# Optimization experiments

Hardware: AMD Instinct MI355X
Metric: run time of the kernel (lower is better)

The kernel has to match this reference:

```python
import jax, jax.numpy as jnp
import numpy as np

B, T, NI, NH, NO = 32, 2048, 1, 512, 1


def setup_inputs() -> dict:
    key = jax.random.key(0)
    ks = jax.random.split(key, 7)
    x = jax.random.normal(ks[0], (B, T, NI), dtype=jnp.float32)
    # torch code draws h_0 ~ U[-1,1) once and tiles over batch; here per-batch uniform
    h_0 = jax.random.uniform(ks[1], (B, NH), dtype=jnp.float32) * 2.0 - 1.0
    w_input_std = 1.0 / np.sqrt(NH)
    W_ih = jax.random.normal(ks[2], (NH, NI), dtype=jnp.float32) * w_input_std
    prob_c = 0.1
    w_hidden_std = 1.5 / np.sqrt(prob_c * NH)
    mask = jax.random.bernoulli(ks[3], prob_c, (NH, NH)).astype(jnp.float32)
    W_hh = jax.random.normal(ks[4], (NH, NH), dtype=jnp.float32) * w_hidden_std * mask
    W_hz = jax.random.normal(ks[5], (NO, NH), dtype=jnp.float32) * w_input_std
    W_zh = jax.random.uniform(ks[6], (NH, NO), dtype=jnp.float32, minval=-1.0, maxval=1.0)
    return {"x": x, "h_0": h_0, "W_ih": W_ih, "W_hh": W_hh, "W_hz": W_hz, "W_zh": W_zh}


def reference(x, h_0, W_ih, W_hh, W_hz, W_zh):
    dt, tau = 0.001, 0.01
    alpha = dt / tau  # 0.1
    # precompute input projection for all timesteps: [T, B, NH]
    x_proj = jnp.einsum('bti,hi->tbh', x, W_ih)

    def step(carry, xp_t):
        h_prev, z_prev = carry  # [B,NH], [B,NO]
        h_transfer = jnp.tanh(h_prev)
        dhdt = -h_prev + h_transfer @ W_hh.T + xp_t + z_prev @ W_zh.T
        h_t = h_prev + alpha * dhdt
        z_t = jnp.tanh(h_t) @ W_hz.T
        return (h_t, z_t), (h_t, z_t)

    z0 = jnp.tanh(h_0) @ W_hz.T
    _, (h, z) = jax.lax.scan(step, (h_0, z0), x_proj)
    # scan stacks time first -> [T,B,*]; transpose to [B,T,*]
    return jnp.swapaxes(z, 0, 1), jnp.swapaxes(h, 0, 1)
```

## Files before the change

### kernel.cpp

```cpp
#include <hip/hip_runtime.h>


#define NH   512
#define TT   2048
#define BB   32
#define PAD  96
#define PIN  64

__global__ __launch_bounds__(512) void count_nnz(
    const float* __restrict__ Whh, int* __restrict__ nnz) {
  const int wib  = threadIdx.x >> 6;
  const int lane = threadIdx.x & 63;
  const int row  = blockIdx.x * 8 + wib;
  const float* wrow = Whh + (size_t)row * NH;
  int cnt = 0;
  for (int c = 0; c < NH / 64; ++c)
    cnt += __popcll(__ballot(wrow[c * 64 + lane] != 0.0f));
  if (lane == 0) nnz[row] = cnt;
}

__global__ __launch_bounds__(512) void sort_rows(
    const int* __restrict__ nnz, int* __restrict__ perm) {
  __shared__ int nl[NH];
  const int j = threadIdx.x;
  const int my = nnz[j];
  nl[j] = my;
  __syncthreads();
  int r = 0;
  const int4* p4 = (const int4*)nl;
  for (int i = 0; i < NH / 4; ++i) {
    int4 v = p4[i];
    const int base = i * 4;
    r += (v.x > my) || (v.x == my && base + 0 < j);
    r += (v.y > my) || (v.y == my && base + 1 < j);
    r += (v.z > my) || (v.z == my && base + 2 < j);
    r += (v.w > my) || (v.w == my && base + 3 < j);
  }
  perm[r] = j;
}

__global__ __launch_bounds__(64) void build_schedule(
    const float* __restrict__ Whh, const int* __restrict__ perm,
    float* __restrict__ vals, unsigned* __restrict__ offs,
    int* __restrict__ cntw) {
  __shared__ int cnt[2][32];
  const int lane = threadIdx.x;
  const int wid  = blockIdx.x;
  const int p    = wid * 64 + lane;
  const int half = lane >> 5;
  const int home = lane & 31;
  const int row  = perm[p];
  const float* wrow = Whh + (size_t)row * NH;

  unsigned occ32[16];
  int remaining = 0;
  unsigned nonempty = 0;
  #pragma unroll
  for (int r = 0; r < 16; ++r) {
    unsigned lo = 0, hi = 0;
    #pragma unroll
    for (int m = 0; m < 16; ++m) {
      lo |= (wrow[(2 * r)     + 32 * m] != 0.f) ? (1u << m) : 0u;
      hi |= (wrow[(2 * r + 1) + 32 * m] != 0.f) ? (1u << m) : 0u;
    }
    occ32[r] = lo | (hi << 16);
    remaining += __popc(lo) + __popc(hi);
    if (lo) nonempty |= 1u << (2 * r);
    if (hi) nonempty |= 1u << (2 * r + 1);
  }

  int s = 0;
  while (__ballot(remaining > 0) != 0ull && s < PAD) {
    cnt[half][home] = 0;
    __builtin_amdgcn_wave_barrier();

    bool placed = false;
    int  mybank = 0;
    unsigned excl = 0;

    for (int round = 0; round < 10; ++round) {
      const int cap = (round < 3) ? 1 : 2;
      if (round == 3) excl = 0;
      unsigned cand = (placed || remaining == 0) ? 0u : (nonempty & ~excl);
      bool want = cand != 0u;
      int bl = 0;
      if (want) {
        unsigned rot = home ? ((cand >> home) | (cand << (32 - home))) : cand;
        bl = (home + __ffs(rot) - 1) & 31;
      }
      if (__ballot(want) == 0ull) break;
      if (want) {
        int old = atomicAdd(&cnt[half][bl], 1);
        if (old < cap) { placed = true; mybank = bl; }
        else { atomicSub(&cnt[half][bl], 1); excl |= 1u << bl; }
      }
      __builtin_amdgcn_wave_barrier();
    }

    if (!placed && remaining > 0 && (PAD - s) <= remaining) {
      placed = true;
      mybank = __ffs(nonempty) - 1;
    }

    float v = 0.f; unsigned col = 0u;
    if (placed) {
      #pragma unroll
      for (int r = 0; r < 16; ++r) {
        if (r == (mybank >> 1)) {
          unsigned w   = occ32[r];
          unsigned m16 = (mybank & 1) ? (w >> 16) : (w & 0xFFFFu);
          int m = __ffs(m16) - 1;
          col = (unsigned)(mybank + 32 * m);
          unsigned nm = m16 & (m16 - 1u);
          occ32[r] = (mybank & 1) ? ((w & 0x0000FFFFu) | (nm << 16))
                                  : ((w & 0xFFFF0000u) | nm);
          if (nm == 0u) nonempty &= ~(1u << mybank);
        }
      }
      v = wrow[col];
      --remaining;
    }
    vals[s * NH + p] = v;
    offs[s * NH + p] = col;
    ++s;
  }
  if (lane == 0) cntw[wid] = s;
  for (int e = s; e < PAD; ++e) {
    vals[e * NH + p] = 0.f;
    offs[e * NH + p] = 0u;
  }
}

template <int CTRL, int RM>
__device__ __forceinline__ float dppadd(float v) {
  int t = __builtin_amdgcn_update_dpp(0, __float_as_int(v), CTRL, RM, 0xF, true);
  return v + __int_as_float(t);
}
__device__ __forceinline__ float wave_sum_lane63(float v) {
  v = dppadd<0xB1,  0xF>(v);
  v = dppadd<0x4E,  0xF>(v);
  v = dppadd<0x141, 0xF>(v);
  v = dppadd<0x140, 0xF>(v);
  v = dppadd<0x142, 0xA>(v);
  v = dppadd<0x143, 0xC>(v);
  return v;
}

__device__ __forceinline__ float ftanh(float x) {
  float xc = fminf(9.0f, fmaxf(-9.0f, x));
  float t  = __expf(2.0f * xc);
  return (t - 1.0f) * __builtin_amdgcn_rcpf(t + 1.0f);
}

#define GA(T_RD, E) (*(const float*)((const char*)(T_RD) + cidx[E]))

#define ESN_STEP(T_RD, T_WR, RWR, SIDX)                                      \
  {                                                                          \
    float d0 = 0.f, d1 = 0.f, d2 = 0.f, d3 = 0.f;                            \
    _Pragma("unroll")                                                        \
    for (int e = 0; e < PAD; e += 4) {                                       \
      if (e < cw) {                                                          \
        d0 = fmaf(wval[e + 0], GA(T_RD, e + 0), d0);                         \
        d1 = fmaf(wval[e + 1], GA(T_RD, e + 1), d1);                         \
        d2 = fmaf(wval[e + 2], GA(T_RD, e + 2), d2);                         \
        d3 = fmaf(wval[e + 3], GA(T_RD, e + 3), d3);                         \
      }                                                                      \
    }                                                                        \
    float dot  = (d0 + d1) + (d2 + d3);                                      \
    float xp   = x_lds[SIDX] * w_ih;                                         \
    float dhdt = ((dot - h) + xp) + z_prev * w_zh;                           \
    float hn   = h + 0.1f * dhdt;                                            \
    float thn  = ftanh(hn);                                                  \
    T_WR[row] = thn;                                                         \
    oh[(SIDX) * NH + row] = hn;                                              \
    float pzs = wave_sum_lane63(thn * w_hz);                                 \
    if (lane == 63) red[RWR][wid] = pzs;                                     \
    asm volatile("s_waitcnt lgkmcnt(0)\n\ts_barrier" ::: "memory");          \
    float4 r0 = *(const float4*)&red[RWR][0];                                \
    float4 r1 = *(const float4*)&red[RWR][4];                                \
    float z = ((r0.x + r0.y) + (r0.z + r0.w)) + ((r1.x + r1.y) + (r1.z + r1.w)); \
    if (p == 0) oz[SIDX] = z;                                                \
    z_prev = z; h = hn;                                                      \
  }

__global__ __launch_bounds__(512, 2) void esn_steps(
    const float* __restrict__ x,   const float* __restrict__ h0,
    const float* __restrict__ Wih, const float* __restrict__ Whz,
    const float* __restrict__ Wzh, const float* __restrict__ vals,
    const unsigned* __restrict__ offs, const int* __restrict__ perm,
    const int* __restrict__ cntw, float* __restrict__ out) {
  __shared__ float t_lds[2][NH];
  __shared__ float x_lds[TT];
  __shared__ __align__(16) float red[2][8];

  const int p    = threadIdx.x;
  const int b    = blockIdx.x;
  const int lane = p & 63;
  const int wid  = p >> 6;
  const int row  = perm[p];

  float* t0 = t_lds[0];
  float* t1 = t_lds[1];

  for (int i = p; i < TT; i += NH) x_lds[i] = x[(size_t)b * TT + i];

  int cw = __builtin_amdgcn_readfirstlane((cntw[wid] + 3) & ~3);

  float    wval[PAD];
  unsigned cidx[PAD];
  #pragma unroll
  for (int e = 0; e < PAD; ++e) {
    wval[e] = vals[e * NH + p];
    cidx[e] = offs[e * NH + p] * 4u;
  }
  #pragma unroll
  for (int e = 0; e < PIN; ++e)
    asm volatile("" : "+v"(wval[e]), "+v"(cidx[e]));

  const float w_ih = Wih[row];
  const float w_hz = Whz[row];
  const float w_zh = Wzh[row];
  float h = h0[(size_t)b * NH + row];

  float* oz = out + (size_t)b * TT;
  float* oh = out + (size_t)BB * TT + (size_t)b * TT * NH;

  float th0 = ftanh(h);
  t0[row] = th0;
  float pz = wave_sum_lane63(th0 * w_hz);
  if (lane == 63) red[0][wid] = pz;
  __syncthreads();
  float4 i0 = *(const float4*)&red[0][0];
  float4 i1 = *(const float4*)&red[0][4];
  float z_prev = ((i0.x + i0.y) + (i0.z + i0.w)) + ((i1.x + i1.y) + (i1.z + i1.w));

  for (int s = 0; s < TT; s += 2) {
    ESN_STEP(t0, t1, 1, s);
    ESN_STEP(t1, t0, 0, s + 1);
  }
}

extern "C" void kernel_launch(void* const* d_in, const int* in_sizes, int n_in,
                              void* d_out, int out_size, void* d_ws,
                              size_t ws_size, hipStream_t stream) {
  const float* x   = (const float*)d_in[0];
  const float* h0  = (const float*)d_in[1];
  const float* Wih = (const float*)d_in[2];
  const float* Whh = (const float*)d_in[3];
  const float* Whz = (const float*)d_in[4];
  const float* Wzh = (const float*)d_in[5];
  float* out = (float*)d_out;

  float*    vals = (float*)d_ws;
  unsigned* offs = (unsigned*)(vals + PAD * NH);
  int*      nnz  = (int*)(offs + PAD * NH);
  int*      perm = nnz + NH;
  int*      cntw = perm + NH;

  hipLaunchKernelGGL(count_nnz, dim3(NH / 8), dim3(512), 0, stream, Whh, nnz);
  hipLaunchKernelGGL(sort_rows, dim3(1), dim3(512), 0, stream, nnz, perm);
  hipLaunchKernelGGL(build_schedule, dim3(8), dim3(64), 0, stream,
                     Whh, perm, vals, offs, cntw);
  hipLaunchKernelGGL(esn_steps, dim3(BB), dim3(512), 0, stream,
                     x, h0, Wih, Whz, Wzh, vals, offs, perm, cntw, out);
}
```

Measured before the change: 2.795 ms.

## Split each batch recurrence across four workgroups with tagged global exchange

Each batch element is now handled by four 128-thread workgroups, each owning two waves' worth of rows, instead of one 512-thread block. The tanh state and partial z sums are exchanged through global memory each step using tag-stamped 64-bit relaxed atomics with spin-polling and double buffering. Block indices are mapped so that the four workgroups of a batch land on the same XCD. The intent is to spread the per-step dot-product work over more CUs and lower per-step latency, at the cost of a cross-workgroup global-memory handshake every step. Correctness depends on all 128 workgroups being co-resident, and the buffers are not reset between calls.

New measurement: 4.421 ms. +58.2%, slower.

```diff
diff --git a/kernel.cpp b/kernel.cpp
--- a/kernel.cpp
+++ b/kernel.cpp
@@ -4,8 +4,12 @@
 #define NH   512
 #define TT   2048
 #define BB   32
+#define SQ   4
+#define TPB  128
 #define PAD  96
-#define PIN  64
+#define PIN  96
+
+typedef unsigned long long u64;
 
 __global__ __launch_bounds__(512) void count_nnz(
     const float* __restrict__ Whh, int* __restrict__ nnz) {
@@ -152,59 +156,76 @@
   return (t - 1.0f) * __builtin_amdgcn_rcpf(t + 1.0f);
 }
 
+__device__ __forceinline__ u64 aload(u64* p) {
+  return __hip_atomic_load(p, __ATOMIC_RELAXED, __HIP_MEMORY_SCOPE_AGENT);
+}
+__device__ __forceinline__ void astore(u64* p, u64 v) {
+  __hip_atomic_store(p, v, __ATOMIC_RELAXED, __HIP_MEMORY_SCOPE_AGENT);
+}
+
 #define GA(T_RD, E) (*(const float*)((const char*)(T_RD) + cidx[E]))
 
-#define ESN_STEP(T_RD, T_WR, RWR, SIDX)                                      \
+#define EXCHANGE(TB, ZQ, TAG, DO_OZ, SIDX)                                   \
   {                                                                          \
-    float d0 = 0.f, d1 = 0.f, d2 = 0.f, d3 = 0.f;                            \
-    _Pragma("unroll")                                                        \
-    for (int e = 0; e < PAD; e += 4) {                                       \
-      if (e < cw) {                                                          \
-        d0 = fmaf(wval[e + 0], GA(T_RD, e + 0), d0);                         \
-        d1 = fmaf(wval[e + 1], GA(T_RD, e + 1), d1);                         \
-        d2 = fmaf(wval[e + 2], GA(T_RD, e + 2), d2);                         \
-        d3 = fmaf(wval[e + 3], GA(T_RD, e + 3), d3);                         \
-      }                                                                      \
+    asm volatile("s_waitcnt lgkmcnt(0)\n\ts_barrier" ::: "memory");          \
+    if (t == 0)                                                              \
+      astore((ZQ) + q, ((u64)(TAG) << 32) |                                  \
+                       (u64)__float_as_uint(red[0] + red[1]));               \
+    u64 v0=0, v1=0, v2=0, v3=0, vz=0;                                        \
+    bool o0=false, o1=false, o2=false, o3=false, ok_z = (t >= 4);            \
+    for (;;) {                                                               \
+      if (!o0)   v0 = aload((TB) + t);                                       \
+      if (!o1)   v1 = aload((TB) + t + 128);                                 \
+      if (!o2)   v2 = aload((TB) + t + 256);                                 \
+      if (!o3)   v3 = aload((TB) + t + 384);                                 \
+      if (!ok_z) vz = aload((ZQ) + t);                                       \
+      o0 = (unsigned)(v0 >> 32) == (TAG);                                    \
+      o1 = (unsigned)(v1 >> 32) == (TAG);                                    \
+      o2 = (unsigned)(v2 >> 32) == (TAG);                                    \
+      o3 = (unsigned)(v3 >> 32) == (TAG);                                    \
+      ok_z = ok_z || ((unsigned)(vz >> 32) == (TAG));                        \
+      if (o0 & o1 & o2 & o3 & ok_z) break;                                   \
     }                                                                        \
-    float dot  = (d0 + d1) + (d2 + d3);                                      \
-    float xp   = x_lds[SIDX] * w_ih;                                         \
-    float dhdt = ((dot - h) + xp) + z_prev * w_zh;                           \
-    float hn   = h + 0.1f * dhdt;                                            \
-    float thn  = ftanh(hn);                                                  \
-    T_WR[row] = thn;                                                         \
-    oh[(SIDX) * NH + row] = hn;                                              \
-    float pzs = wave_sum_lane63(thn * w_hz);                                 \
-    if (lane == 63) red[RWR][wid] = pzs;                                     \
+    tl[t]       = __uint_as_float((unsigned)v0);                             \
+    tl[t + 128] = __uint_as_float((unsigned)v1);                             \
+    tl[t + 256] = __uint_as_float((unsigned)v2);                             \
+    tl[t + 384] = __uint_as_float((unsigned)v3);                             \
+    if (w == 0) {                                                            \
+      float zv = (t < 4) ? __uint_as_float((unsigned)vz) : 0.0f;             \
+      float zz = (__shfl(zv, 0) + __shfl(zv, 1)) +                           \
+                 (__shfl(zv, 2) + __shfl(zv, 3));                            \
+      if (t == 0) { zbc = zz; if ((DO_OZ) && q == 0) oz[SIDX] = zz; }        \
+    }                                                                        \
     asm volatile("s_waitcnt lgkmcnt(0)\n\ts_barrier" ::: "memory");          \
-    float4 r0 = *(const float4*)&red[RWR][0];                                \
-    float4 r1 = *(const float4*)&red[RWR][4];                                \
-    float z = ((r0.x + r0.y) + (r0.z + r0.w)) + ((r1.x + r1.y) + (r1.z + r1.w)); \
-    if (p == 0) oz[SIDX] = z;                                                \
-    z_prev = z; h = hn;                                                      \
-  }
-
-__global__ __launch_bounds__(512, 2) void esn_steps(
+    z_prev = zbc;                                                            \
+  }
+
+__global__ __launch_bounds__(TPB, 1) void esn_split(
     const float* __restrict__ x,   const float* __restrict__ h0,
     const float* __restrict__ Wih, const float* __restrict__ Whz,
     const float* __restrict__ Wzh, const float* __restrict__ vals,
     const unsigned* __restrict__ offs, const int* __restrict__ perm,
-    const int* __restrict__ cntw, float* __restrict__ out) {
-  __shared__ float t_lds[2][NH];
+    const int* __restrict__ cntw, u64* __restrict__ tbuf,
+    u64* __restrict__ zq, float* __restrict__ out) {
+  __shared__ float tl[NH];
   __shared__ float x_lds[TT];
-  __shared__ __align__(16) float red[2][8];
-
-  const int p    = threadIdx.x;
-  const int b    = blockIdx.x;
-  const int lane = p & 63;
-  const int wid  = p >> 6;
-  const int row  = perm[p];
-
-  float* t0 = t_lds[0];
-  float* t1 = t_lds[1];
-
-  for (int i = p; i < TT; i += NH) x_lds[i] = x[(size_t)b * TT + i];
-
-  int cw = __builtin_amdgcn_readfirstlane((cntw[wid] + 3) & ~3);
+  __shared__ float red[2];
+  __shared__ float zbc;
+
+  const int t    = threadIdx.x;
+  const int w    = t >> 6;
+  const int lane = t & 63;
+  const int bid = blockIdx.x;
+  const int xcd = bid & 7, sl = bid >> 3;
+  const int b   = xcd * 4 + (sl >> 2);
+  const int q   = sl & 3;
+  const int g   = (w == 0) ? q : (7 - q);
+  const int p   = g * 64 + lane;
+  const int row = perm[p];
+
+  for (int i = t; i < TT; i += TPB) x_lds[i] = x[(size_t)b * TT + i];
+
+  int cw = __builtin_amdgcn_readfirstlane((cntw[g] + 3) & ~3);
 
   float    wval[PAD];
   unsigned cidx[PAD];
@@ -221,22 +242,50 @@
   const float w_hz = Whz[row];
   const float w_zh = Wzh[row];
   float h = h0[(size_t)b * NH + row];
+  float z_prev;
 
   float* oz = out + (size_t)b * TT;
   float* oh = out + (size_t)BB * TT + (size_t)b * TT * NH;
 
-  float th0 = ftanh(h);
-  t0[row] = th0;
-  float pz = wave_sum_lane63(th0 * w_hz);
-  if (lane == 63) red[0][wid] = pz;
-  __syncthreads();
-  float4 i0 = *(const float4*)&red[0][0];
-  float4 i1 = *(const float4*)&red[0][4];
-  float z_prev = ((i0.x + i0.y) + (i0.z + i0.w)) + ((i1.x + i1.y) + (i1.z + i1.w));
-
-  for (int s = 0; s < TT; s += 2) {
-    ESN_STEP(t0, t1, 1, s);
-    ESN_STEP(t1, t0, 0, s + 1);
+  {
+    float thn = ftanh(h);
+    u64* tb  = tbuf + (size_t)b * NH;
+    u64* zqb = zq   + (size_t)b * SQ;
+    astore(tb + row, ((u64)1u << 32) | (u64)__float_as_uint(thn));
+    float pzs = wave_sum_lane63(thn * w_hz);
+    if (lane == 63) red[w] = pzs;
+    EXCHANGE(tb, zqb, 1u, false, 0)
+  }
+
+  for (int s = 0; s < TT; ++s) {
+    float d0 = 0.f, d1 = 0.f, d2 = 0.f, d3 = 0.f;
+    #pragma unroll
+    for (int e = 0; e < PAD; e += 4) {
+      if (e < cw) {
+        d0 = fmaf(wval[e + 0], GA(tl, e + 0), d0);
+        d1 = fmaf(wval[e + 1], GA(tl, e + 1), d1);
+        d2 = fmaf(wval[e + 2], GA(tl, e + 2), d2);
+        d3 = fmaf(wval[e + 3], GA(tl, e + 3), d3);
+      }
+    }
+    float dot  = (d0 + d1) + (d2 + d3);
+
+    float xp   = x_lds[s] * w_ih;
+    float dhdt = ((dot - h) + xp) + z_prev * w_zh;
+    float hn   = h + 0.1f * dhdt;
+    __builtin_nontemporal_store(hn, &oh[(size_t)s * NH + row]);
+    float thn  = ftanh(hn);
+
+    const unsigned tg = (unsigned)(s + 2);
+    const int buf = (s + 1) & 1;
+    u64* tb  = tbuf + ((size_t)buf * BB + b) * NH;
+    u64* zqb = zq   + ((size_t)buf * BB + b) * SQ;
+    astore(tb + row, ((u64)tg << 32) | (u64)__float_as_uint(thn));
+    float pzs = wave_sum_lane63(thn * w_hz);
+    if (lane == 63) red[w] = pzs;
+
+    EXCHANGE(tb, zqb, tg, true, s)
+    h = hn;
   }
 }
 
@@ -251,16 +300,20 @@
   const float* Wzh = (const float*)d_in[5];
   float* out = (float*)d_out;
 
-  float*    vals = (float*)d_ws;
-  unsigned* offs = (unsigned*)(vals + PAD * NH);
-  int*      nnz  = (int*)(offs + PAD * NH);
-  int*      perm = nnz + NH;
-  int*      cntw = perm + NH;
+  char* ws = (char*)d_ws;
+  float*    vals = (float*)ws;
+  unsigned* offs = (unsigned*)(ws + 196608);
+  int*      nnz  = (int*)(ws + 393216);
+  int*      perm = (int*)(ws + 395264);
+  int*      cntw = (int*)(ws + 397312);
+  u64*      tbuf = (u64*)(ws + 397376);
+  u64*      zqb  = (u64*)(ws + 659520);
 
   hipLaunchKernelGGL(count_nnz, dim3(NH / 8), dim3(512), 0, stream, Whh, nnz);
   hipLaunchKernelGGL(sort_rows, dim3(1), dim3(512), 0, stream, nnz, perm);
   hipLaunchKernelGGL(build_schedule, dim3(8), dim3(64), 0, stream,
                      Whh, perm, vals, offs, cntw);
-  hipLaunchKernelGGL(esn_steps, dim3(BB), dim3(512), 0, stream,
-                     x, h0, Wih, Whz, Wzh, vals, offs, perm, cntw, out);
-}
+  hipLaunchKernelGGL(esn_split, dim3(BB * SQ), dim3(TPB), 0, stream,
+                     x, h0, Wih, Whz, Wzh, vals, offs, perm, cntw,
+                     tbuf, zqb, out);
+}
```
